# Kernel tuning notes

Measured on AMD Instinct MI355X. Metric: run time of the kernel, lower is better.

The kernel has to match this reference:

```python
import jax, jax.numpy as jnp
import numpy as np

N_HEADS = 16
DIM = 1024
BS, SLEN = 2, 2048
EPS = 1e-12  # F.normalize eps


def setup_inputs() -> dict:
    key = jax.random.key(0)
    ks = jax.random.split(key, 10)
    d = DIM
    inp = {
        "x": jax.random.normal(ks[0], (BS, SLEN, d), dtype=jnp.float32),
        # causal attention mask, as produced by get_masks(causal=True)
        "mask": jnp.tril(jnp.ones((SLEN, SLEN), dtype=bool))[None].repeat(BS, axis=0),
        "Wq": jax.random.normal(ks[1], (d, d), dtype=jnp.float32) / np.sqrt(d),
        "bq": jax.random.normal(ks[2], (d,), dtype=jnp.float32) * 0.02,
        "Wk": jax.random.normal(ks[3], (d, d), dtype=jnp.float32) / np.sqrt(d),
        "bk": jax.random.normal(ks[4], (d,), dtype=jnp.float32) * 0.02,
        "Wv": jax.random.normal(ks[5], (d, d), dtype=jnp.float32) / np.sqrt(d),
        "bv": jax.random.normal(ks[6], (d,), dtype=jnp.float32) * 0.02,
        "Wo": jax.random.normal(ks[7], (d, d), dtype=jnp.float32) / np.sqrt(d),
        "bo": jax.random.normal(ks[8], (d,), dtype=jnp.float32) * 0.02,
        # learnable scale for normalized (cosine) attention
        "attention_scale": jnp.ones((1,), dtype=jnp.float32) / np.sqrt(d // N_HEADS),
    }
    return inp


def _shape(t, bs, h, dph):
    # (bs, len, dim) -> (bs, h, len, dph)
    return t.reshape(bs, -1, h, dph).transpose(0, 2, 1, 3)


def reference(x, mask, Wq, bq, Wk, bk, Wv, bv, Wo, bo, attention_scale):
    bs, qlen, dim = x.shape
    h = N_HEADS
    dph = dim // h

    q = _shape(x @ Wq + bq, bs, h, dph)  # (bs, h, qlen, dph)
    k = _shape(x @ Wk + bk, bs, h, dph)
    v = _shape(x @ Wv + bv, bs, h, dph)

    # normalized (cosine) attention: L2-normalize q and k, learned scale
    q = q / jnp.maximum(jnp.linalg.norm(q, axis=-1, keepdims=True), EPS)
    k = k / jnp.maximum(jnp.linalg.norm(k, axis=-1, keepdims=True), EPS)
    q = q * attention_scale

    scores = jnp.einsum("bhqd,bhkd->bhqk", q, k)  # (bs, h, qlen, klen)
    scores = jnp.where(mask[:, None, :, :], scores, -jnp.inf)
    weights = jax.nn.softmax(scores, axis=-1)

    ctx = jnp.einsum("bhqk,bhkd->bhqd", weights, v)
    ctx = ctx.transpose(0, 2, 1, 3).reshape(bs, qlen, dim)
    return ctx @ Wo + bo
```

## Files before the change

kernel.cpp:

```cpp
#include <hip/hip_runtime.h>
#include <math.h>

#define NH 16
#define DPH 64
#define SLEN 2048
#define BSZ 2
#define DIM 1024
#define NTOK (BSZ * SLEN)
#define LOG2E 1.44269504088896f

typedef unsigned short ushortT;
typedef __attribute__((ext_vector_type(8))) short short8;
typedef __attribute__((ext_vector_type(4))) short s16x4;
typedef __attribute__((ext_vector_type(4))) float f32x4;

typedef __attribute__((address_space(1))) const unsigned int gu32c;
typedef __attribute__((address_space(3))) unsigned int lu32;

__device__ __forceinline__ void gld16(const void* g, void* l) {
    __builtin_amdgcn_global_load_lds((gu32c*)g, (lu32*)l, 16, 0, 0);
}

__device__ __forceinline__ ushortT f2bf(float f) {
    unsigned int u = __builtin_bit_cast(unsigned int, f);
    u = u + 0x7fffu + ((u >> 16) & 1u);
    return (ushortT)(u >> 16);
}

__global__ __launch_bounds__(256) void cvt_x(const float* __restrict__ x,
                                             ushortT* __restrict__ xb) {
    size_t i = (size_t)blockIdx.x * 256 + threadIdx.x;
    float4 a = *(const float4*)&x[i * 8];
    float4 b = *(const float4*)&x[i * 8 + 4];
    short8 v;
    v[0] = (short)f2bf(a.x); v[1] = (short)f2bf(a.y);
    v[2] = (short)f2bf(a.z); v[3] = (short)f2bf(a.w);
    v[4] = (short)f2bf(b.x); v[5] = (short)f2bf(b.y);
    v[6] = (short)f2bf(b.z); v[7] = (short)f2bf(b.w);
    *(short8*)&xb[i * 8] = v;
}

__global__ __launch_bounds__(256) void cvt_wt(const float* __restrict__ W0, const float* __restrict__ W1,
                                              const float* __restrict__ W2, const float* __restrict__ W3,
                                              ushortT* __restrict__ T0, ushortT* __restrict__ T1,
                                              ushortT* __restrict__ T2, ushortT* __restrict__ T3) {
    const float* W = blockIdx.z == 0 ? W0 : blockIdx.z == 1 ? W1 : blockIdx.z == 2 ? W2 : W3;
    ushortT* T = blockIdx.z == 0 ? T0 : blockIdx.z == 1 ? T1 : blockIdx.z == 2 ? T2 : T3;
    __shared__ float tile[64][65];
    const int tid = threadIdx.x;
    const int kb = blockIdx.y * 64, nb = blockIdx.x * 64;
#pragma unroll
    for (int it = 0; it < 4; it++) {
        int chunk = it * 256 + tid;
        int r = chunk >> 4, c4 = (chunk & 15) * 4;
        *(float4*)&tile[r][c4] = *(const float4*)&W[(size_t)(kb + r) * DIM + nb + c4];
    }
    __syncthreads();
#pragma unroll
    for (int it = 0; it < 2; it++) {
        int chunk = it * 256 + tid;
        int n = chunk >> 3, k8 = (chunk & 7) * 8;
        short8 o;
#pragma unroll
        for (int j = 0; j < 8; j++) o[j] = (short)f2bf(tile[k8 + j][n]);
        *(short8*)&T[(size_t)(nb + n) * DIM + kb + k8] = o;
    }
}

__global__ __launch_bounds__(256) void gemm_qkv(const ushortT* __restrict__ A,
                                                const ushortT* __restrict__ Bt,
                                                const float* __restrict__ bq,
                                                const float* __restrict__ bk,
                                                const float* __restrict__ bv,
                                                const float* __restrict__ ascale,
                                                ushortT* __restrict__ Qb,
                                                ushortT* __restrict__ Kb,
                                                ushortT* __restrict__ VF) {
    __shared__ __align__(16) ushortT As[128 * 64];
    __shared__ __align__(16) ushortT Bs[128 * 64];
    const int tid = threadIdx.x;
    const int lane = tid & 63, wid = tid >> 6;
    const int wr = wid >> 1, wc = wid & 1;
    const int lo = lane & 15, hi = lane >> 4;
    const int row0 = blockIdx.y * 128, col0 = blockIdx.x * 128;
    const int r8 = lane >> 3, sp = lane & 7;
    const int srcoff = (sp ^ r8) << 3;
    f32x4 acc[4][4] = {};

    for (int kc = 0; kc < DIM; kc += 64) {
        __syncthreads();
#pragma unroll
        for (int it = 0; it < 4; it++) {
            int seg = it * 4 + wid;
            int row = seg * 8 + r8;
            gld16(&A[(size_t)(row0 + row) * DIM + kc + srcoff], &As[seg * 512]);
            gld16(&Bt[(size_t)(col0 + row) * DIM + kc + srcoff], &Bs[seg * 512]);
        }
        __syncthreads();
#pragma unroll
        for (int ks = 0; ks < 2; ks++) {
            short8 af[4], bfr[4];
#pragma unroll
            for (int m = 0; m < 4; m++) {
                int row = wr * 64 + m * 16 + lo;
                af[m] = *(const short8*)&As[row * 64 + (((ks * 4 + hi) ^ (row & 7)) << 3)];
            }
#pragma unroll
            for (int n = 0; n < 4; n++) {
                int row = wc * 64 + n * 16 + lo;
                bfr[n] = *(const short8*)&Bs[row * 64 + (((ks * 4 + hi) ^ (row & 7)) << 3)];
            }
#pragma unroll
            for (int m = 0; m < 4; m++)
#pragma unroll
                for (int n = 0; n < 4; n++)
                    acc[m][n] = __builtin_amdgcn_mfma_f32_16x16x32_bf16(af[m], bfr[n], acc[m][n], 0, 0, 0);
        }
    }

    const int cg = col0 + wc * 64;
    const int which = cg >> 10;
    const int cwin = cg & 1023;
    const int h = cwin >> 6;
    const int t0g = row0 + wr * 64;
    const int b = t0g >> 11, tok0 = t0g & (SLEN - 1);
    const float* bias = which == 0 ? bq : which == 1 ? bk : bv;

    float bb[4];
#pragma unroll
    for (int n = 0; n < 4; n++) bb[n] = bias[cwin + n * 16 + lo];
#pragma unroll
    for (int m = 0; m < 4; m++)
#pragma unroll
        for (int n = 0; n < 4; n++)
#pragma unroll
            for (int r = 0; r < 4; r++) acc[m][n][r] += bb[n];

    if (which < 2) {
        float asc = (which == 0) ? ascale[0] * LOG2E : 1.0f;
#pragma unroll
        for (int m = 0; m < 4; m++)
#pragma unroll
            for (int r = 0; r < 4; r++) {
                float ss = acc[m][0][r] * acc[m][0][r] + acc[m][1][r] * acc[m][1][r] +
                           acc[m][2][r] * acc[m][2][r] + acc[m][3][r] * acc[m][3][r];
#pragma unroll
                for (int o = 8; o > 0; o >>= 1) ss += __shfl_xor(ss, o);
                float sc = asc / fmaxf(sqrtf(ss), 1e-12f);
#pragma unroll
                for (int n = 0; n < 4; n++) acc[m][n][r] *= sc;
            }
    }

    __syncthreads();
    ushortT* tl = (wid < 2) ? &As[wid * 4096] : &Bs[(wid - 2) * 4096];
#pragma unroll
    for (int m = 0; m < 4; m++)
#pragma unroll
        for (int n = 0; n < 4; n++)
#pragma unroll
            for (int r = 0; r < 4; r++) {
                int row = m * 16 + hi * 4 + r;
                int col = n * 16 + lo;
                int cc = col >> 3;
                tl[row * 64 + ((cc ^ (row >> 3)) << 3) + (col & 7)] = f2bf(acc[m][n][r]);
            }

    if (which < 2) {
        ushortT* op = which == 0 ? Qb : Kb;
        const size_t base = ((size_t)(b * NH + h) * SLEN + tok0) * DPH;
#pragma unroll
        for (int j = 0; j < 8; j++) {
            int cid = j * 64 + lane;
            int r2 = cid >> 3, cc = cid & 7;
            uint4 v = *(const uint4*)&tl[r2 * 64 + ((cc ^ (r2 >> 3)) << 3)];
            *(uint4*)&op[base + (size_t)cid * 8] = v;
        }
    } else {
        const int kt = tok0 >> 6;
        const size_t base = ((size_t)(b * NH + h) * 32 + kt) * 4096;
#pragma unroll
        for (int c = 0; c < 8; c++) {
            short8 v;
#pragma unroll
            for (int e = 0; e < 8; e++) {
                int rowL = (c & 1) * 32 + hi * 8 + e;
                int colL = (c >> 1) * 16 + lo;
                int cc2 = colL >> 3;
                v[e] = (short)tl[rowL * 64 + ((cc2 ^ (rowL >> 3)) << 3) + (colL & 7)];
            }
            *(short8*)&VF[base + (size_t)(c * 64 + lane) * 8] = v;
        }
    }
}

__global__ __launch_bounds__(256) void gemm_oproj(const ushortT* __restrict__ A,
                                                  const ushortT* __restrict__ Bt,
                                                  const float* __restrict__ bias,
                                                  float* __restrict__ outF) {
    __shared__ __align__(16) unsigned char lbuf[32768];
    ushortT* As = (ushortT*)lbuf;
    ushortT* Bs = (ushortT*)(lbuf + 8192);
    const int tid = threadIdx.x;
    const int lane = tid & 63, wid = tid >> 6;
    const int wr = wid >> 1, wc = wid & 1;
    const int lo = lane & 15, hi = lane >> 4;
    const int row0 = blockIdx.y * 64, col0 = blockIdx.x * 128;
    const int r8 = lane >> 3, sp = lane & 7;
    const int srcoff = (sp ^ r8) << 3;
    f32x4 acc[2][4] = {};

    for (int kc = 0; kc < DIM; kc += 64) {
        __syncthreads();
#pragma unroll
        for (int it = 0; it < 2; it++) {
            int seg = it * 4 + wid;
            int row = seg * 8 + r8;
            gld16(&A[(size_t)(row0 + row) * DIM + kc + srcoff], &As[seg * 512]);
        }
#pragma unroll
        for (int it = 0; it < 4; it++) {
            int seg = it * 4 + wid;
            int row = seg * 8 + r8;
            gld16(&Bt[(size_t)(col0 + row) * DIM + kc + srcoff], &Bs[seg * 512]);
        }
        __syncthreads();
#pragma unroll
        for (int ks = 0; ks < 2; ks++) {
            short8 af[2], bfr[4];
#pragma unroll
            for (int m = 0; m < 2; m++) {
                int row = wr * 32 + m * 16 + lo;
                af[m] = *(const short8*)&As[row * 64 + (((ks * 4 + hi) ^ (row & 7)) << 3)];
            }
#pragma unroll
            for (int n = 0; n < 4; n++) {
                int row = wc * 64 + n * 16 + lo;
                bfr[n] = *(const short8*)&Bs[row * 64 + (((ks * 4 + hi) ^ (row & 7)) << 3)];
            }
#pragma unroll
            for (int m = 0; m < 2; m++)
#pragma unroll
                for (int n = 0; n < 4; n++)
                    acc[m][n] = __builtin_amdgcn_mfma_f32_16x16x32_bf16(af[m], bfr[n], acc[m][n], 0, 0, 0);
        }
    }

    float bb[4];
#pragma unroll
    for (int n = 0; n < 4; n++) bb[n] = bias[col0 + wc * 64 + n * 16 + lo];
#pragma unroll
    for (int m = 0; m < 2; m++)
#pragma unroll
        for (int n = 0; n < 4; n++)
#pragma unroll
            for (int r = 0; r < 4; r++) acc[m][n][r] += bb[n];

    __syncthreads();
    float* tl = (float*)(lbuf + wid * 8192);
#pragma unroll
    for (int m = 0; m < 2; m++)
#pragma unroll
        for (int n = 0; n < 4; n++)
#pragma unroll
            for (int r = 0; r < 4; r++) {
                int row = m * 16 + hi * 4 + r;
                int col = n * 16 + lo;
                int cc = col >> 2;
                tl[row * 64 + ((cc ^ (row & 7)) << 2) + (col & 3)] = acc[m][n][r];
            }
#pragma unroll
    for (int j = 0; j < 8; j++) {
        int cid = j * 64 + lane;
        int rowR = cid >> 4, cc = cid & 15;
        f32x4 v = *(const f32x4*)&tl[rowR * 64 + ((cc ^ (rowR & 7)) << 2)];
        int rg = row0 + wr * 32 + rowR;
        int cgl = col0 + wc * 64 + cc * 4;
        *(f32x4*)&outF[(size_t)rg * DIM + cgl] = v;
    }
}

__global__ __launch_bounds__(512, 4) void attn(const ushortT* __restrict__ Q,
                                               const ushortT* __restrict__ K,
                                               const ushortT* __restrict__ VF,
                                               const float* __restrict__ scale,
                                               ushortT* __restrict__ ctx) {
    __shared__ __align__(16) ushortT Ks[64 * 64];
    __shared__ __align__(16) ushortT Ps[8 * 16 * 64];
    const int tid = threadIdx.x, lane = tid & 63, wid = tid >> 6;
    const int wg = wid & 3, sg = wid >> 2;
    const int bh = blockIdx.x, p = blockIdx.y;
    const int qt = sg ? p : 31 - p;
    const int kbmax = 31 - p;
    const size_t hb = (size_t)bh * SLEN * DPH;
    const int lo = lane & 15, hi = lane >> 4;
    const float mshift = fabsf(scale[0]) * LOG2E;

    short8 aq[2];
    {
        const int qrow = qt * 64 + wg * 16 + lo;
#pragma unroll
        for (int ks = 0; ks < 2; ks++)
            aq[ks] = *(const short8*)&Q[hb + (size_t)qrow * DPH + ks * 32 + 8 * hi];
    }

    const int srow = tid >> 3, sslot = tid & 7;
    const int sldsoff = srow * 64 + ((sslot ^ (srow & 7)) << 3);
    uint4 kr = *(const uint4*)&K[hb + (size_t)srow * DPH + sslot * 8];
    *(uint4*)&Ks[sldsoff] = kr;
    __syncthreads();

    f32x4 accd[4] = {};
    float lp = 0.f;

    for (int kb = 0; kb <= kbmax; kb++) {
        if (kb < kbmax)
            kr = *(const uint4*)&K[hb + (size_t)((kb + 1) * 64 + srow) * DPH + sslot * 8];

        if (kb <= qt) {
            short8 bv[8];
            const ushortT* vt = &VF[(((size_t)bh * 32 + kb) * 512 + lane) * 8];
#pragma unroll
            for (int c = 0; c < 8; c++) bv[c] = *(const short8*)&vt[(size_t)c * 512];

            f32x4 sf[4] = {};
#pragma unroll
            for (int ks = 0; ks < 2; ks++)
#pragma unroll
                for (int j = 0; j < 4; j++) {
                    int row = j * 16 + lo;
                    short8 bk = *(const short8*)&Ks[row * 64 + (((ks * 4 + hi) ^ (row & 7)) << 3)];
                    sf[j] = __builtin_amdgcn_mfma_f32_16x16x32_bf16(bk, aq[ks], sf[j], 0, 0, 0);
                }

            if (kb == qt) {
#pragma unroll
                for (int j = 0; j < 4; j++)
#pragma unroll
                    for (int r = 0; r < 4; r++)
                        if (j * 16 + 4 * hi + r > wg * 16 + lo) sf[j][r] = -INFINITY;
            }

#pragma unroll
            for (int j = 0; j < 4; j++) {
                s16x4 pk;
#pragma unroll
                for (int r = 0; r < 4; r++) {
                    float pv = __builtin_amdgcn_exp2f(sf[j][r] - mshift);
                    lp += pv;
                    pk[r] = (short)f2bf(pv);
                }
                int slot = (4 * j + hi) ^ (2 * (lo & 7));
                *(s16x4*)&Ps[wid * 1024 + lo * 64 + slot * 4] = pk;
            }

#pragma unroll
            for (int ks = 0; ks < 2; ks++) {
                int slot0 = (8 * ks + 2 * hi) ^ (2 * (lo & 7));
                short8 ap = *(const short8*)&Ps[wid * 1024 + lo * 64 + slot0 * 4];
#pragma unroll
                for (int jd = 0; jd < 4; jd++)
                    accd[jd] = __builtin_amdgcn_mfma_f32_16x16x32_bf16(ap, bv[jd * 2 + ks], accd[jd], 0, 0, 0);
            }
        }

        __syncthreads();
        if (kb < kbmax) {
            *(uint4*)&Ks[sldsoff] = kr;
            __syncthreads();
        }
    }

    lp += __shfl_xor(lp, 16);
    lp += __shfl_xor(lp, 32);

    const int b = bh >> 4, h = bh & 15;
#pragma unroll
    for (int r = 0; r < 4; r++) {
        float lr = __shfl(lp, (lane & 48) | (4 * hi + r));
        float inv = 1.0f / lr;
        int t = qt * 64 + wg * 16 + 4 * hi + r;
#pragma unroll
        for (int jd = 0; jd < 4; jd++) {
            int d = jd * 16 + lo;
            ctx[(size_t)(b * SLEN + t) * DIM + h * 64 + d] = f2bf(accd[jd][r] * inv);
        }
    }
}

extern "C" void kernel_launch(void* const* d_in, const int* in_sizes, int n_in,
                              void* d_out, int out_size, void* d_ws,
                              size_t ws_size, hipStream_t stream) {
    const float* x = (const float*)d_in[0];
    const float* Wq = (const float*)d_in[2];
    const float* bq = (const float*)d_in[3];
    const float* Wk = (const float*)d_in[4];
    const float* bk = (const float*)d_in[5];
    const float* Wv = (const float*)d_in[6];
    const float* bv = (const float*)d_in[7];
    const float* Wo = (const float*)d_in[8];
    const float* bo = (const float*)d_in[9];
    const float* ascale = (const float*)d_in[10];
    float* outF = (float*)d_out;

    unsigned char* ws = (unsigned char*)d_ws;
    const size_t MB = 1u << 20;
    ushortT* xb = (ushortT*)(ws);
    ushortT* Wqkvt = (ushortT*)(ws + 8 * MB);
    ushortT* Wot = (ushortT*)(ws + 14 * MB);
    ushortT* Qb = (ushortT*)(ws + 16 * MB);
    ushortT* Kb = (ushortT*)(ws + 24 * MB);
    ushortT* VFb = (ushortT*)(ws + 32 * MB);
    ushortT* ctxb = (ushortT*)(ws + 40 * MB);

    cvt_x<<<NTOK * DIM / (8 * 256), 256, 0, stream>>>(x, xb);
    cvt_wt<<<dim3(16, 16, 4), 256, 0, stream>>>(Wq, Wk, Wv, Wo, Wqkvt,
                                                Wqkvt + (size_t)1024 * 1024,
                                                Wqkvt + (size_t)2048 * 1024, Wot);

    gemm_qkv<<<dim3(3 * DIM / 128, NTOK / 128), 256, 0, stream>>>(
        xb, Wqkvt, bq, bk, bv, ascale, Qb, Kb, VFb);

    attn<<<dim3(32, 16), 512, 0, stream>>>(Qb, Kb, VFb, ascale, ctxb);

    gemm_oproj<<<dim3(DIM / 128, NTOK / 64), 256, 0, stream>>>(ctxb, Wot, bo, outF);
}
```

Before: 111.8 us.

## Rewrite QKV GEMM with 256x256 tiles, double-buffered LDS and block swizzle

Replaces the 128x128, 4-wave QKV projection GEMM with a 256x256-tile, 8-wave kernel. It double-buffers LDS so the next K-chunk loads while MFMAs run, raises MFMA priority with s_setprio, and remaps block IDs for L2 locality. The larger tile is meant to raise arithmetic intensity and hide global-load latency. The costs are 128KB of LDS per block and only 192 blocks, which may underfill the GPU's CUs.

```diff
diff --git a/kernel.cpp b/kernel.cpp
--- a/kernel.cpp
+++ b/kernel.cpp
@@ -67,79 +67,104 @@
     }
 }
 
-__global__ __launch_bounds__(256) void gemm_qkv(const ushortT* __restrict__ A,
-                                                const ushortT* __restrict__ Bt,
-                                                const float* __restrict__ bq,
-                                                const float* __restrict__ bk,
-                                                const float* __restrict__ bv,
-                                                const float* __restrict__ ascale,
-                                                ushortT* __restrict__ Qb,
-                                                ushortT* __restrict__ Kb,
-                                                ushortT* __restrict__ VF) {
-    __shared__ __align__(16) ushortT As[128 * 64];
-    __shared__ __align__(16) ushortT Bs[128 * 64];
+__device__ __forceinline__ void stage_tile(const ushortT* __restrict__ A,
+                                           const ushortT* __restrict__ Bt,
+                                           ushortT* lds, int row0, int col0,
+                                           int kc, int bb, int srow, int sphys) {
+#pragma unroll
+    for (int h = 0; h < 4; h++) {
+        int rl = (h & 1) * 128 + srow;
+        int lch = sphys ^ (((rl >> 3) & 1) << 1);
+        const ushortT* g = (h < 2) ? &A[(size_t)(row0 + rl) * DIM + kc + lch * 8]
+                                   : &Bt[(size_t)(col0 + rl) * DIM + kc + lch * 8];
+        int lb = ((h < 2) ? 0 : 32768) + bb * 16384 + rl * 32 + sphys * 8;
+        gld16(g, &lds[lb]);
+        gld16(g + 32, &lds[lb + 8192]);
+    }
+}
+
+__global__ __launch_bounds__(512, 2) void gemm_qkv8(const ushortT* __restrict__ A,
+                                                    const ushortT* __restrict__ Bt,
+                                                    const float* __restrict__ bq,
+                                                    const float* __restrict__ bk,
+                                                    const float* __restrict__ bv,
+                                                    const float* __restrict__ ascale,
+                                                    ushortT* __restrict__ Qb,
+                                                    ushortT* __restrict__ Kb,
+                                                    ushortT* __restrict__ VF) {
+    __shared__ __align__(16) ushortT lds[65536];
     const int tid = threadIdx.x;
     const int lane = tid & 63, wid = tid >> 6;
-    const int wr = wid >> 1, wc = wid & 1;
+    const int wm = wid >> 2, wn = wid & 3;
     const int lo = lane & 15, hi = lane >> 4;
-    const int row0 = blockIdx.y * 128, col0 = blockIdx.x * 128;
-    const int r8 = lane >> 3, sp = lane & 7;
-    const int srcoff = (sp ^ r8) << 3;
-    f32x4 acc[4][4] = {};
-
-    for (int kc = 0; kc < DIM; kc += 64) {
-        __syncthreads();
-#pragma unroll
-        for (int it = 0; it < 4; it++) {
-            int seg = it * 4 + wid;
-            int row = seg * 8 + r8;
-            gld16(&A[(size_t)(row0 + row) * DIM + kc + srcoff], &As[seg * 512]);
-            gld16(&Bt[(size_t)(col0 + row) * DIM + kc + srcoff], &Bs[seg * 512]);
-        }
-        __syncthreads();
-#pragma unroll
-        for (int ks = 0; ks < 2; ks++) {
+    const int bid = blockIdx.x;
+    const int swz = (bid & 7) * 24 + (bid >> 3);
+    const int bx = swz % 12, by = swz / 12;
+    const int row0 = by * 256, col0 = bx * 256;
+    const int srow = tid >> 2, sphys = tid & 3;
+    f32x4 acc[8][4] = {};
+
+    stage_tile(A, Bt, lds, row0, col0, 0, 0, srow, sphys);
+
+    for (int tt = 0; tt < 16; ++tt) {
+        const int bb = tt & 1;
+        const int abase = bb * 16384, bbase = 32768 + bb * 16384;
+#pragma unroll
+        for (int ph = 0; ph < 4; ++ph) {
+            const int ks = ph & 1, mh = ph >> 1;
+            if (ph == 0) {
+                asm volatile("s_waitcnt vmcnt(0)" ::: "memory");
+                asm volatile("s_barrier" ::: "memory");
+            }
             short8 af[4], bfr[4];
 #pragma unroll
-            for (int m = 0; m < 4; m++) {
-                int row = wr * 64 + m * 16 + lo;
-                af[m] = *(const short8*)&As[row * 64 + (((ks * 4 + hi) ^ (row & 7)) << 3)];
+            for (int mm = 0; mm < 4; mm++) {
+                int row = wm * 128 + (mh * 4 + mm) * 16 + lo;
+                int phys = hi ^ (((row >> 3) & 1) << 1);
+                af[mm] = *(const short8*)&lds[abase + ks * 8192 + row * 32 + phys * 8];
             }
 #pragma unroll
             for (int n = 0; n < 4; n++) {
-                int row = wc * 64 + n * 16 + lo;
-                bfr[n] = *(const short8*)&Bs[row * 64 + (((ks * 4 + hi) ^ (row & 7)) << 3)];
-            }
-#pragma unroll
-            for (int m = 0; m < 4; m++)
+                int row = wn * 64 + n * 16 + lo;
+                int phys = hi ^ (((row >> 3) & 1) << 1);
+                bfr[n] = *(const short8*)&lds[bbase + ks * 8192 + row * 32 + phys * 8];
+            }
+            if (ph == 0 && tt < 15)
+                stage_tile(A, Bt, lds, row0, col0, (tt + 1) * 64, bb ^ 1, srow, sphys);
+            __builtin_amdgcn_s_setprio(1);
+#pragma unroll
+            for (int mm = 0; mm < 4; mm++)
 #pragma unroll
                 for (int n = 0; n < 4; n++)
-                    acc[m][n] = __builtin_amdgcn_mfma_f32_16x16x32_bf16(af[m], bfr[n], acc[m][n], 0, 0, 0);
-        }
-    }
-
-    const int cg = col0 + wc * 64;
+                    acc[mh * 4 + mm][n] = __builtin_amdgcn_mfma_f32_16x16x32_bf16(
+                        af[mm], bfr[n], acc[mh * 4 + mm][n], 0, 0, 0);
+            __builtin_amdgcn_s_setprio(0);
+            asm volatile("s_barrier" ::: "memory");
+        }
+    }
+
+    const int cg = col0 + wn * 64;
     const int which = cg >> 10;
     const int cwin = cg & 1023;
     const int h = cwin >> 6;
-    const int t0g = row0 + wr * 64;
+    const int t0g = row0 + wm * 128;
     const int b = t0g >> 11, tok0 = t0g & (SLEN - 1);
     const float* bias = which == 0 ? bq : which == 1 ? bk : bv;
 
-    float bb[4];
-#pragma unroll
-    for (int n = 0; n < 4; n++) bb[n] = bias[cwin + n * 16 + lo];
-#pragma unroll
-    for (int m = 0; m < 4; m++)
+    float bb4[4];
+#pragma unroll
+    for (int n = 0; n < 4; n++) bb4[n] = bias[cwin + n * 16 + lo];
+#pragma unroll
+    for (int m = 0; m < 8; m++)
 #pragma unroll
         for (int n = 0; n < 4; n++)
 #pragma unroll
-            for (int r = 0; r < 4; r++) acc[m][n][r] += bb[n];
+            for (int r = 0; r < 4; r++) acc[m][n][r] += bb4[n];
 
     if (which < 2) {
         float asc = (which == 0) ? ascale[0] * LOG2E : 1.0f;
 #pragma unroll
-        for (int m = 0; m < 4; m++)
+        for (int m = 0; m < 8; m++)
 #pragma unroll
             for (int r = 0; r < 4; r++) {
                 float ss = acc[m][0][r] * acc[m][0][r] + acc[m][1][r] * acc[m][1][r] +
@@ -152,44 +177,54 @@
             }
     }
 
-    __syncthreads();
-    ushortT* tl = (wid < 2) ? &As[wid * 4096] : &Bs[(wid - 2) * 4096];
-#pragma unroll
-    for (int m = 0; m < 4; m++)
-#pragma unroll
-        for (int n = 0; n < 4; n++)
-#pragma unroll
-            for (int r = 0; r < 4; r++) {
-                int row = m * 16 + hi * 4 + r;
-                int col = n * 16 + lo;
-                int cc = col >> 3;
-                tl[row * 64 + ((cc ^ (row >> 3)) << 3) + (col & 7)] = f2bf(acc[m][n][r]);
-            }
-
+    ushortT* tl = &lds[wid * 8192];
     if (which < 2) {
+#pragma unroll
+        for (int m = 0; m < 8; m++)
+#pragma unroll
+            for (int n = 0; n < 4; n++)
+#pragma unroll
+                for (int r = 0; r < 4; r++) {
+                    int row = m * 16 + 4 * hi + r;
+                    int c = n * 2 + (lo >> 3);
+                    tl[row * 64 + ((c ^ (row & 7)) << 3) + (lo & 7)] = f2bf(acc[m][n][r]);
+                }
         ushortT* op = which == 0 ? Qb : Kb;
         const size_t base = ((size_t)(b * NH + h) * SLEN + tok0) * DPH;
 #pragma unroll
-        for (int j = 0; j < 8; j++) {
+        for (int j = 0; j < 16; j++) {
             int cid = j * 64 + lane;
-            int r2 = cid >> 3, cc = cid & 7;
-            uint4 v = *(const uint4*)&tl[r2 * 64 + ((cc ^ (r2 >> 3)) << 3)];
+            int rowL = cid >> 3, c = cid & 7;
+            uint4 v = *(const uint4*)&tl[rowL * 64 + ((c ^ (rowL & 7)) << 3)];
             *(uint4*)&op[base + (size_t)cid * 8] = v;
         }
     } else {
-        const int kt = tok0 >> 6;
-        const size_t base = ((size_t)(b * NH + h) * 32 + kt) * 4096;
-#pragma unroll
-        for (int c = 0; c < 8; c++) {
+#pragma unroll
+        for (int m = 0; m < 8; m++)
+#pragma unroll
+            for (int n = 0; n < 4; n++)
+#pragma unroll
+                for (int r = 0; r < 4; r++) {
+                    int row = m * 16 + 4 * hi + r;
+                    int c = n * 2 + (lo >> 3);
+                    tl[row * 64 + ((c ^ ((row >> 3) & 7)) << 3) + (lo & 7)] = f2bf(acc[m][n][r]);
+                }
+        const int bh = b * NH + h;
+        const int kt0 = tok0 >> 6;
+#pragma unroll
+        for (int i = 0; i < 16; i++) {
+            int kk = i >> 3;
+            int c = i & 7;
+            int jd = c >> 1, ks2 = c & 1;
+            int colL = jd * 16 + lo;
+            int c2 = colL >> 3;
             short8 v;
 #pragma unroll
             for (int e = 0; e < 8; e++) {
-                int rowL = (c & 1) * 32 + hi * 8 + e;
-                int colL = (c >> 1) * 16 + lo;
-                int cc2 = colL >> 3;
-                v[e] = (short)tl[rowL * 64 + ((cc2 ^ (rowL >> 3)) << 3) + (colL & 7)];
-            }
-            *(short8*)&VF[base + (size_t)(c * 64 + lane) * 8] = v;
+                int rowL = kk * 64 + ks2 * 32 + 8 * hi + e;
+                v[e] = (short)tl[rowL * 64 + ((c2 ^ ((rowL >> 3) & 7)) << 3) + (colL & 7)];
+            }
+            *(short8*)&VF[((size_t)bh * 32 + kt0 + kk) * 4096 + (size_t)(c * 64 + lane) * 8] = v;
         }
     }
 }
@@ -418,8 +453,7 @@
                                                 Wqkvt + (size_t)1024 * 1024,
                                                 Wqkvt + (size_t)2048 * 1024, Wot);
 
-    gemm_qkv<<<dim3(3 * DIM / 128, NTOK / 128), 256, 0, stream>>>(
-        xb, Wqkvt, bq, bk, bv, ascale, Qb, Kb, VFb);
+    gemm_qkv8<<<dim3(192), 512, 0, stream>>>(xb, Wqkvt, bq, bk, bv, ascale, Qb, Kb, VFb);
 
     attn<<<dim3(32, 16), 512, 0, stream>>>(Qb, Kb, VFb, ascale, ctxb);
 
```

Result: faster. 106.8 us (-4.5%).
